# Performance work log

Hardware: AMD Instinct MI355X
Metric: run time of the kernel (lower is better)

## Reference

```python
import jax, jax.numpy as jnp
import numpy as np

N = 50000      # nodes
E = 400000     # edges (avg degree 8)
G = 64         # graphs in batch
IN_DIM = 128
OUT_DIM = 16


def _linear_params(key, fan_in, fan_out):
    k1, k2 = jax.random.split(key)
    s = 1.0 / np.sqrt(fan_in)
    W = jax.random.uniform(k1, (fan_in, fan_out), minval=-s, maxval=s, dtype=jnp.float32)
    b = jax.random.uniform(k2, (fan_out,), minval=-s, maxval=s, dtype=jnp.float32)
    return W, b


def setup_inputs() -> dict:
    key = jax.random.key(0)
    ks = jax.random.split(key, 12)
    x = jax.random.normal(ks[0], (N, IN_DIM), dtype=jnp.float32)
    edge_index = jax.random.randint(ks[1], (2, E), 0, N)
    # balanced graph assignment (sorted, every graph id present)
    batch = (jnp.arange(N) * G) // N
    W1, b1 = _linear_params(ks[2], IN_DIM, 64)
    W2, b2 = _linear_params(ks[3], 64, 256)
    W3, b3 = _linear_params(ks[4], 256, 512)
    W4, b4 = _linear_params(ks[5], 512, 64)
    Wr, br = _linear_params(ks[6], IN_DIM, 64)
    fc1_W, fc1_b = _linear_params(ks[7], 64, 64)
    fc2_W, fc2_b = _linear_params(ks[8], 64, OUT_DIM)
    ln_g = jnp.ones((64,), jnp.float32); ln_b = jnp.zeros((64,), jnp.float32)
    fcn_g = jnp.ones((64,), jnp.float32); fcn_b = jnp.zeros((64,), jnp.float32)
    return dict(x=x, edge_index=edge_index, batch=batch,
                W1=W1, b1=b1, W2=W2, b2=b2, W3=W3, b3=b3, W4=W4, b4=b4,
                Wr=Wr, br=br, ln_g=ln_g, ln_b=ln_b,
                fc1_W=fc1_W, fc1_b=fc1_b, fcn_g=fcn_g, fcn_b=fcn_b,
                fc2_W=fc2_W, fc2_b=fc2_b)


def _leaky_relu(h):
    return jnp.where(h >= 0, h, 0.01 * h)


def _layer_norm(h, g, b, eps=1e-5):
    m = jnp.mean(h, axis=-1, keepdims=True)
    v = jnp.var(h, axis=-1, keepdims=True)
    return (h - m) * jax.lax.rsqrt(v + eps) * g + b


def reference(x, edge_index, batch, W1, b1, W2, b2, W3, b3, W4, b4,
              Wr, br, ln_g, ln_b, fc1_W, fc1_b, fcn_g, fcn_b, fc2_W, fc2_b):
    src, dst = edge_index[0], edge_index[1]
    n = x.shape[0]
    # PyG GCNConv normalization with self-loops: deg = 1 + in-degree
    deg = jax.ops.segment_sum(jnp.ones(src.shape[0], x.dtype), dst, num_segments=n) + 1.0
    dis = jax.lax.rsqrt(deg)                 # [N]
    edge_norm = (dis[src] * dis[dst])[:, None]   # [E,1]
    self_norm = (dis * dis)[:, None]             # [N,1]

    def gcn_conv(h, W, b):
        h = h @ W                                            # transform first (PyG order)
        agg = jax.ops.segment_sum(h[src] * edge_norm, dst, num_segments=n)
        return agg + h * self_norm + b                       # self-loop term + bias

    residual = x @ Wr + br
    h = _leaky_relu(gcn_conv(x, W1, b1))
    h = _leaky_relu(gcn_conv(h, W2, b2))
    h = _leaky_relu(gcn_conv(h, W3, b3))
    h = _leaky_relu(gcn_conv(h, W4, b4))
    h = _layer_norm(h + residual, ln_g, ln_b)
    # global max pool over graphs
    p = jax.ops.segment_max(h, batch, num_segments=G)        # [G,64]
    p = _layer_norm(p @ fc1_W + fc1_b, fcn_g, fcn_b)
    p = _leaky_relu(p)
    return p @ fc2_W + fc2_b                                 # [G,16]
```

## Files before the change

kernel.cpp:

```cpp
#include <hip/hip_runtime.h>
#include <hip/hip_bf16.h>
#include <math.h>

typedef short bf16x8 __attribute__((ext_vector_type(8)));
typedef short bf16x4 __attribute__((ext_vector_type(4)));
typedef float f32x4 __attribute__((ext_vector_type(4)));

__device__ inline unsigned short f2bf(float f) {
  unsigned u = __float_as_uint(f);
  u += 0x7FFF + ((u >> 16) & 1);
  return (unsigned short)(u >> 16);
}
__device__ inline float bf2f(unsigned short h) {
  return __uint_as_float(((unsigned)h) << 16);
}
__device__ inline float bflo(unsigned u) { return __uint_as_float(u << 16); }
__device__ inline float bfhi(unsigned u) { return __uint_as_float(u & 0xffff0000u); }


__global__ __launch_bounds__(256) void count_k(const int* __restrict__ dst, int* __restrict__ cnt, int e) {
  int i = blockIdx.x * 256 + threadIdx.x;
  if (i < e) atomicAdd(&cnt[dst[i]], 1);
}

__global__ __launch_bounds__(256) void scan_a(const int* __restrict__ cnt, int* __restrict__ bsum, int n) {
  int i = blockIdx.x * 256 + threadIdx.x;
  int v = (i < n) ? cnt[i] : 0;
#pragma unroll
  for (int o = 32; o > 0; o >>= 1) v += __shfl_xor(v, o);
  __shared__ int ws[4];
  if ((threadIdx.x & 63) == 0) ws[threadIdx.x >> 6] = v;
  __syncthreads();
  if (threadIdx.x == 0) bsum[blockIdx.x] = ws[0] + ws[1] + ws[2] + ws[3];
}

__global__ __launch_bounds__(256) void scan_b(const int* __restrict__ bsum, int* __restrict__ bpre,
                                              int* __restrict__ off_n, int nb) {
  __shared__ int s[256];
  int t = threadIdx.x;
  int v = (t < nb) ? bsum[t] : 0;
  s[t] = v;
  __syncthreads();
  for (int o = 1; o < 256; o <<= 1) {
    int u = (t >= o) ? s[t - o] : 0;
    __syncthreads();
    s[t] += u;
    __syncthreads();
  }
  if (t < nb) bpre[t] = s[t] - v;
  if (t == 255) off_n[0] = s[255];
}

__global__ __launch_bounds__(256) void scan_c(const int* __restrict__ cnt, const int* __restrict__ bpre,
                                              int* __restrict__ off, int* __restrict__ cursor,
                                              float* __restrict__ dis, int n) {
  __shared__ int s[256];
  int i = blockIdx.x * 256 + threadIdx.x;
  int t = threadIdx.x;
  int v = (i < n) ? cnt[i] : 0;
  s[t] = v;
  __syncthreads();
  for (int o = 1; o < 256; o <<= 1) {
    int u = (t >= o) ? s[t - o] : 0;
    __syncthreads();
    s[t] += u;
    __syncthreads();
  }
  if (i < n) {
    int ov = bpre[blockIdx.x] + s[t] - v;
    off[i] = ov;
    cursor[i] = ov;
    dis[i] = rsqrtf((float)v + 1.0f);
  }
}

__global__ __launch_bounds__(256) void scatter_k(const int* __restrict__ src, const int* __restrict__ dst,
                                                 int* __restrict__ cursor, int* __restrict__ csr, int e) {
  int i = blockIdx.x * 256 + threadIdx.x;
  if (i < e) {
    int p = atomicAdd(&cursor[dst[i]], 1);
    csr[p] = src[i];
  }
}


__global__ __launch_bounds__(256) void wconv_k(const float* __restrict__ W1, const float* __restrict__ Wr,
                                               const float* __restrict__ W2, const float* __restrict__ W3,
                                               const float* __restrict__ W4,
                                               short* __restrict__ o1, short* __restrict__ oR,
                                               short* __restrict__ o2, short* __restrict__ o3,
                                               short* __restrict__ o4) {
  int b = blockIdx.x;
  const float* W; short* O; int K, N, nr;
  if (b < 64)       { W = W1; O = o1; K = 128; N = 64;  nr = b; }
  else if (b < 128) { W = Wr; O = oR; K = 128; N = 64;  nr = b - 64; }
  else if (b < 384) { W = W2; O = o2; K = 64;  N = 256; nr = b - 128; }
  else if (b < 896) { W = W3; O = o3; K = 256; N = 512; nr = b - 384; }
  else              { W = W4; O = o4; K = 512; N = 64;  nr = b - 896; }
  for (int k = threadIdx.x; k < K; k += 256)
    O[(size_t)nr * K + k] = (short)f2bf(W[(size_t)k * N + nr]);
}


template<int KT, int NTOT, int WM, int WN, int BIAS, int RELU, int ABF, int OBF, int SPLIT, int SCL, int BLK>
__global__ __launch_bounds__(256, BLK) void mgemm(const void* __restrict__ Av,
                                                  const short* __restrict__ Wc,
                                                  const float* __restrict__ bias,
                                                  void* __restrict__ Cv, void* __restrict__ Cv2,
                                                  const float* __restrict__ scl, int M) {
  __shared__ short As[64 * WM][ABF ? 40 : 72];
  __shared__ short Bs[64 * WN][40];
  const int tid = threadIdx.x;
  const int row0 = blockIdx.x * (64 * WM);
  const int col0 = blockIdx.y * (64 * WN);
  const int w = tid >> 6, lane = tid & 63;
  const int wm = w / WN, wn = w % WN;
  const int rm = wm * 64, cn = wn * 64;
  const int lm = lane & 15, lk = (lane >> 4) * 8;

  f32x4 acc[4][4];
#pragma unroll
  for (int i = 0; i < 4; i++)
#pragma unroll
    for (int j = 0; j < 4; j++)
#pragma unroll
      for (int r = 0; r < 4; r++) acc[i][j][r] = 0.f;

  for (int k0 = 0; k0 < KT; k0 += 32) {
#pragma unroll
    for (int p = 0; p < WM; p++) {
      int r = (tid >> 2) + p * 64;
      int kseg = (tid & 3) * 8;
      int gr = row0 + r;
      if (ABF) {
        bf16x8 v = {0, 0, 0, 0, 0, 0, 0, 0};
        if (gr < M) v = *(const bf16x8*)((const short*)Av + (size_t)gr * KT + k0 + kseg);
        *(bf16x8*)&As[r][kseg] = v;
      } else {
        float4 v0 = {0.f, 0.f, 0.f, 0.f}, v1 = {0.f, 0.f, 0.f, 0.f};
        if (gr < M) {
          const float* ap = (const float*)Av + (size_t)gr * KT + k0 + kseg;
          v0 = *(const float4*)ap;
          v1 = *(const float4*)(ap + 4);
        }
        float vv[8] = {v0.x, v0.y, v0.z, v0.w, v1.x, v1.y, v1.z, v1.w};
        bf16x8 hv, lv;
#pragma unroll
        for (int j = 0; j < 8; j++) {
          unsigned short h = f2bf(vv[j]);
          hv[j] = (short)h;
          lv[j] = (short)f2bf(vv[j] - bf2f(h));
        }
        *(bf16x8*)&As[r][kseg] = hv;
        *(bf16x8*)&As[r][32 + kseg] = lv;
      }
    }
#pragma unroll
    for (int p = 0; p < WN; p++) {
      int nr = (tid >> 2) + p * 64;
      int seg = (tid & 3) * 8;
      *(bf16x8*)&Bs[nr][seg] = *(const bf16x8*)(Wc + (size_t)(col0 + nr) * KT + k0 + seg);
    }
    __syncthreads();

    bf16x8 ah[4], al[4], bb[4];
#pragma unroll
    for (int mt = 0; mt < 4; mt++) {
      ah[mt] = *(const bf16x8*)&As[rm + mt * 16 + lm][lk];
      if (!ABF) al[mt] = *(const bf16x8*)&As[rm + mt * 16 + lm][32 + lk];
    }
#pragma unroll
    for (int nt = 0; nt < 4; nt++) bb[nt] = *(const bf16x8*)&Bs[cn + nt * 16 + lm][lk];
#pragma unroll
    for (int mt = 0; mt < 4; mt++)
#pragma unroll
      for (int nt = 0; nt < 4; nt++) {
        acc[mt][nt] = __builtin_amdgcn_mfma_f32_16x16x32_bf16(ah[mt], bb[nt], acc[mt][nt], 0, 0, 0);
        if (!ABF)
          acc[mt][nt] = __builtin_amdgcn_mfma_f32_16x16x32_bf16(al[mt], bb[nt], acc[mt][nt], 0, 0, 0);
      }
    __syncthreads();
  }

  if (SPLIT) {
    short* epi = (short*)&As[0][0];
    if (wn == 0) {
#pragma unroll
      for (int mt = 0; mt < 4; mt++) {
        int lr = rm + mt * 16 + (lane >> 4) * 4;
#pragma unroll
        for (int r = 0; r < 4; r++) {
          int gr = row0 + lr + r;
          float sc = (SCL && gr < M) ? scl[gr] : 0.f;
#pragma unroll
          for (int nt = 0; nt < 4; nt++)
            epi[(lr + r) * 64 + nt * 16 + lm] = (short)f2bf(acc[mt][nt][r] * sc);
        }
      }
    } else {
#pragma unroll
      for (int mt = 0; mt < 4; mt++) {
        int grb = row0 + rm + mt * 16 + (lane >> 4) * 4;
#pragma unroll
        for (int nt = 0; nt < 4; nt++) {
          int gc = nt * 16 + lm;
          float bv = bias[gc];
#pragma unroll
          for (int r = 0; r < 4; r++) {
            int gr = grb + r;
            if (gr < M) ((float*)Cv2)[(size_t)gr * 64 + gc] = acc[mt][nt][r] + bv;
          }
        }
      }
    }
    __syncthreads();
    int base = tid * 32;
    int row = base >> 6, col = base & 63;
    int gr = row0 + row;
    if (gr < M) {
#pragma unroll
      for (int q = 0; q < 4; q++)
        *(bf16x8*)((short*)Cv + (size_t)gr * 64 + col + q * 8) = *(bf16x8*)&epi[base + q * 8];
    }
  } else if (OBF && WM == 1) {
    short* epi = &Bs[0][0];
    const int NCOL = 64 * WN;
    float bvv[4];
#pragma unroll
    for (int nt = 0; nt < 4; nt++) bvv[nt] = BIAS ? bias[col0 + cn + nt * 16 + lm] : 0.f;
#pragma unroll
    for (int mt = 0; mt < 4; mt++) {
      __syncthreads();
#pragma unroll
      for (int r = 0; r < 4; r++) {
        int gr = row0 + mt * 16 + (lane >> 4) * 4 + r;
        float sc = (SCL && gr < M) ? scl[gr] : 1.f;
#pragma unroll
        for (int nt = 0; nt < 4; nt++) {
          float v = acc[mt][nt][r] + bvv[nt];
          if (RELU) v = (v >= 0.f) ? v : 0.01f * v;
          if (SCL) v *= sc;
          epi[((lane >> 4) * 4 + r) * NCOL + cn + nt * 16 + lm] = (short)f2bf(v);
        }
      }
      __syncthreads();
      const int per = (16 * NCOL) / 256;
      int base = tid * per;
      int lr = base / NCOL, lc = base % NCOL;
      int gr = row0 + mt * 16 + lr;
      if (gr < M) {
#pragma unroll
        for (int q = 0; q < per / 8; q++)
          *(bf16x8*)((short*)Cv + (size_t)gr * NTOT + col0 + lc + q * 8) = *(bf16x8*)&epi[base + q * 8];
      }
    }
  } else {
#pragma unroll
    for (int mt = 0; mt < 4; mt++) {
      int grb = row0 + rm + mt * 16 + (lane >> 4) * 4;
#pragma unroll
      for (int nt = 0; nt < 4; nt++) {
        int gc = col0 + cn + nt * 16 + lm;
        float bv = BIAS ? bias[gc] : 0.f;
#pragma unroll
        for (int r = 0; r < 4; r++) {
          int gr = grb + r;
          if (gr < M) {
            float v = acc[mt][nt][r] + bv;
            if (RELU) v = (v >= 0.f) ? v : 0.01f * v;
            if (SCL) v *= scl[gr];
            if (OBF) ((short*)Cv)[(size_t)gr * NTOT + gc] = (short)f2bf(v);
            else     ((float*)Cv)[(size_t)gr * NTOT + gc] = v;
          }
        }
      }
    }
  }
}


__global__ __launch_bounds__(256, 3) void fused34_k(const short* __restrict__ h2,
                                                    const int* __restrict__ off, const int* __restrict__ csr,
                                                    const short* __restrict__ W3c,
                                                    const float* __restrict__ b3,
                                                    const short* __restrict__ W4c,
                                                    const float* __restrict__ dis,
                                                    short* __restrict__ T4, int M) {
  __shared__ short Bs[2][32][264];
  __shared__ short Ws4[2][64][40];
  __shared__ short Hs[64][40];
  const int tid = threadIdx.x;
  const int row0 = blockIdx.x * 64;
  const int w = tid >> 6, lane = tid & 63;
  const int lm = lane & 15, lk = (lane >> 4) * 8;
  const int rquad = (lane >> 4) * 4;
  const int w4row = tid >> 2, w4seg = (tid & 3) * 8;
  const int qtr = lane >> 4, ql = lane & 15;

  short* Zs = (short*)&Bs[0][0][0];
  for (int pass = 0; pass < 4; pass++) {
    int nid = pass * 16 + w * 4 + qtr;
    int gr = row0 + nid;
    float a[16];
    if (gr < M) {
      float di = dis[gr];
      int e0 = off[gr], e1 = off[gr + 1];
      const short* base = h2 + (size_t)gr * 256 + ql * 16;
      bf16x8 s0 = *(const bf16x8*)base;
      bf16x8 s1 = *(const bf16x8*)(base + 8);
#pragma unroll
      for (int j = 0; j < 8; j++) { a[j] = bf2f((unsigned short)s0[j]); a[8 + j] = bf2f((unsigned short)s1[j]); }
      int e = e0;
      for (; e + 4 <= e1; e += 4) {
        const short* p0 = h2 + (size_t)csr[e]     * 256 + ql * 16;
        const short* p1 = h2 + (size_t)csr[e + 1] * 256 + ql * 16;
        const short* p2 = h2 + (size_t)csr[e + 2] * 256 + ql * 16;
        const short* p3 = h2 + (size_t)csr[e + 3] * 256 + ql * 16;
        bf16x8 t00 = *(const bf16x8*)p0, t01 = *(const bf16x8*)(p0 + 8);
        bf16x8 t10 = *(const bf16x8*)p1, t11 = *(const bf16x8*)(p1 + 8);
        bf16x8 t20 = *(const bf16x8*)p2, t21 = *(const bf16x8*)(p2 + 8);
        bf16x8 t30 = *(const bf16x8*)p3, t31 = *(const bf16x8*)(p3 + 8);
#pragma unroll
        for (int j = 0; j < 8; j++) {
          a[j] += (bf2f((unsigned short)t00[j]) + bf2f((unsigned short)t10[j])) +
                  (bf2f((unsigned short)t20[j]) + bf2f((unsigned short)t30[j]));
          a[8 + j] += (bf2f((unsigned short)t01[j]) + bf2f((unsigned short)t11[j])) +
                      (bf2f((unsigned short)t21[j]) + bf2f((unsigned short)t31[j]));
        }
      }
      for (; e < e1; e++) {
        const short* p = h2 + (size_t)csr[e] * 256 + ql * 16;
        bf16x8 t0 = *(const bf16x8*)p, t1 = *(const bf16x8*)(p + 8);
#pragma unroll
        for (int j = 0; j < 8; j++) {
          a[j] += bf2f((unsigned short)t0[j]);
          a[8 + j] += bf2f((unsigned short)t1[j]);
        }
      }
#pragma unroll
      for (int j = 0; j < 16; j++) a[j] *= di;
    } else {
#pragma unroll
      for (int j = 0; j < 16; j++) a[j] = 0.f;
    }
    bf16x8 o0, o1;
#pragma unroll
    for (int j = 0; j < 8; j++) {
      o0[j] = (short)f2bf(a[j]);
      o1[j] = (short)f2bf(a[8 + j]);
    }
    *(bf16x8*)&Zs[nid * 264 + ql * 16] = o0;
    *(bf16x8*)&Zs[nid * 264 + ql * 16 + 8] = o1;
  }
  __syncthreads();

  bf16x8 afr[8];
  {
    int lr = w * 16 + lm;
#pragma unroll
    for (int kc = 0; kc < 8; kc++)
      afr[kc] = *(const bf16x8*)&Zs[lr * 264 + kc * 32 + lk];
  }
  __syncthreads();

  f32x4 t4acc[4];
#pragma unroll
  for (int nt = 0; nt < 4; nt++)
#pragma unroll
    for (int r = 0; r < 4; r++) t4acc[nt][r] = 0.f;

  bf16x8 pw3[4];
  bf16x8 pw4;
#pragma unroll
  for (int q = 0; q < 4; q++) {
    int flat = q * 2048 + tid * 8;
    pw3[q] = *(const bf16x8*)(W3c + flat);
  }
  pw4 = *(const bf16x8*)(W4c + (size_t)w4row * 512 + w4seg);
#pragma unroll
  for (int q = 0; q < 4; q++) {
    int flat = q * 2048 + tid * 8;
    *(bf16x8*)&Bs[0][flat >> 8][flat & 255] = pw3[q];
  }
  *(bf16x8*)&Ws4[0][w4row][w4seg] = pw4;
  __syncthreads();

  for (int c = 0; c < 16; c++) {
    int cur = c & 1, nxt = cur ^ 1;
    if (c < 15) {
#pragma unroll
      for (int q = 0; q < 4; q++) {
        int flat = q * 2048 + tid * 8;
        pw3[q] = *(const bf16x8*)(W3c + (size_t)(c + 1) * 32 * 256 + flat);
      }
      pw4 = *(const bf16x8*)(W4c + (size_t)w4row * 512 + (c + 1) * 32 + w4seg);
    }

    f32x4 acc1[2];
#pragma unroll
    for (int nt = 0; nt < 2; nt++)
#pragma unroll
      for (int r = 0; r < 4; r++) acc1[nt][r] = 0.f;
#pragma unroll
    for (int k0 = 0; k0 < 8; k0++) {
      bf16x8 bb[2];
#pragma unroll
      for (int nt = 0; nt < 2; nt++) bb[nt] = *(const bf16x8*)&Bs[cur][nt * 16 + lm][k0 * 32 + lk];
#pragma unroll
      for (int nt = 0; nt < 2; nt++)
        acc1[nt] = __builtin_amdgcn_mfma_f32_16x16x32_bf16(afr[k0], bb[nt], acc1[nt], 0, 0, 0);
    }
#pragma unroll
    for (int nt = 0; nt < 2; nt++) {
      float bv = b3[c * 32 + nt * 16 + lm];
#pragma unroll
      for (int r = 0; r < 4; r++) {
        float v = acc1[nt][r] + bv;
        v = (v >= 0.f) ? v : 0.01f * v;
        Hs[w * 16 + rquad + r][nt * 16 + lm] = (short)f2bf(v);
      }
    }
    {
      bf16x8 ah2 = *(const bf16x8*)&Hs[w * 16 + lm][lk];
      bf16x8 bb2[4];
#pragma unroll
      for (int nt = 0; nt < 4; nt++) bb2[nt] = *(const bf16x8*)&Ws4[cur][nt * 16 + lm][lk];
#pragma unroll
      for (int nt = 0; nt < 4; nt++)
        t4acc[nt] = __builtin_amdgcn_mfma_f32_16x16x32_bf16(ah2, bb2[nt], t4acc[nt], 0, 0, 0);
    }
    if (c < 15) {
#pragma unroll
      for (int q = 0; q < 4; q++) {
        int flat = q * 2048 + tid * 8;
        *(bf16x8*)&Bs[nxt][flat >> 8][flat & 255] = pw3[q];
      }
      *(bf16x8*)&Ws4[nxt][w4row][w4seg] = pw4;
    }
    __syncthreads();
  }
  short* epi = (short*)&Bs[0][0][0];
#pragma unroll
  for (int r = 0; r < 4; r++) {
    int lr = w * 16 + rquad + r;
    int gr = row0 + lr;
    float sc = (gr < M) ? dis[gr] : 0.f;
#pragma unroll
    for (int nt = 0; nt < 4; nt++)
      epi[lr * 64 + nt * 16 + lm] = (short)f2bf(t4acc[nt][r] * sc);
  }
  __syncthreads();
  {
    int base = tid * 16;
    int row = base >> 6, col = base & 63;
    int gr = row0 + row;
    if (gr < M) {
      *(bf16x8*)(T4 + (size_t)gr * 64 + col)     = *(bf16x8*)&epi[base];
      *(bf16x8*)(T4 + (size_t)gr * 64 + col + 8) = *(bf16x8*)&epi[base + 8];
    }
  }
}


template<int BR, int OSCL>
__global__ __launch_bounds__(256) void aggb64_k(const short* __restrict__ T, const float* __restrict__ dis,
                                                const int* __restrict__ off, const int* __restrict__ csr,
                                                const float* __restrict__ bias, short* __restrict__ Out, int n) {
  int wv = (blockIdx.x * 256 + threadIdx.x) >> 6;
  int lane = threadIdx.x & 63;
  int qtr = lane >> 4, ql = lane & 15;
  int wid = wv * 4 + qtr;
  if (wid >= n) return;
  float di = dis[wid];
  int e0 = off[wid], e1 = off[wid + 1];
  const uint2* Tw = (const uint2*)T;
  uint2 su = Tw[(size_t)wid * 16 + ql];
  float a0 = bflo(su.x), a1 = bfhi(su.x), a2 = bflo(su.y), a3 = bfhi(su.y);
  int e = e0;
  for (; e + 8 <= e1; e += 8) {
    uint2 u0 = Tw[(size_t)csr[e]     * 16 + ql];
    uint2 u1 = Tw[(size_t)csr[e + 1] * 16 + ql];
    uint2 u2 = Tw[(size_t)csr[e + 2] * 16 + ql];
    uint2 u3 = Tw[(size_t)csr[e + 3] * 16 + ql];
    uint2 u4 = Tw[(size_t)csr[e + 4] * 16 + ql];
    uint2 u5 = Tw[(size_t)csr[e + 5] * 16 + ql];
    uint2 u6 = Tw[(size_t)csr[e + 6] * 16 + ql];
    uint2 u7 = Tw[(size_t)csr[e + 7] * 16 + ql];
    a0 += ((bflo(u0.x) + bflo(u1.x)) + (bflo(u2.x) + bflo(u3.x))) +
          ((bflo(u4.x) + bflo(u5.x)) + (bflo(u6.x) + bflo(u7.x)));
    a1 += ((bfhi(u0.x) + bfhi(u1.x)) + (bfhi(u2.x) + bfhi(u3.x))) +
          ((bfhi(u4.x) + bfhi(u5.x)) + (bfhi(u6.x) + bfhi(u7.x)));
    a2 += ((bflo(u0.y) + bflo(u1.y)) + (bflo(u2.y) + bflo(u3.y))) +
          ((bflo(u4.y) + bflo(u5.y)) + (bflo(u6.y) + bflo(u7.y)));
    a3 += ((bfhi(u0.y) + bfhi(u1.y)) + (bfhi(u2.y) + bfhi(u3.y))) +
          ((bfhi(u4.y) + bfhi(u5.y)) + (bfhi(u6.y) + bfhi(u7.y)));
  }
  for (; e + 4 <= e1; e += 4) {
    uint2 u0 = Tw[(size_t)csr[e]     * 16 + ql];
    uint2 u1 = Tw[(size_t)csr[e + 1] * 16 + ql];
    uint2 u2 = Tw[(size_t)csr[e + 2] * 16 + ql];
    uint2 u3 = Tw[(size_t)csr[e + 3] * 16 + ql];
    a0 += (bflo(u0.x) + bflo(u1.x)) + (bflo(u2.x) + bflo(u3.x));
    a1 += (bfhi(u0.x) + bfhi(u1.x)) + (bfhi(u2.x) + bfhi(u3.x));
    a2 += (bflo(u0.y) + bflo(u1.y)) + (bflo(u2.y) + bflo(u3.y));
    a3 += (bfhi(u0.y) + bfhi(u1.y)) + (bfhi(u2.y) + bfhi(u3.y));
  }
  for (; e < e1; e++) {
    uint2 u = Tw[(size_t)csr[e] * 16 + ql];
    a0 += bflo(u.x); a1 += bfhi(u.x); a2 += bflo(u.y); a3 += bfhi(u.y);
  }
  float v0 = di * a0, v1 = di * a1, v2 = di * a2, v3 = di * a3;
  if (BR) {
    v0 += bias[ql * 4];     v1 += bias[ql * 4 + 1];
    v2 += bias[ql * 4 + 2]; v3 += bias[ql * 4 + 3];
    v0 = (v0 >= 0.f) ? v0 : 0.01f * v0;
    v1 = (v1 >= 0.f) ? v1 : 0.01f * v1;
    v2 = (v2 >= 0.f) ? v2 : 0.01f * v2;
    v3 = (v3 >= 0.f) ? v3 : 0.01f * v3;
  }
  if (OSCL) { v0 *= di; v1 *= di; v2 *= di; v3 *= di; }
  uint2 o;
  o.x = (unsigned)f2bf(v0) | ((unsigned)f2bf(v1) << 16);
  o.y = (unsigned)f2bf(v2) | ((unsigned)f2bf(v3) << 16);
  ((uint2*)Out)[(size_t)wid * 16 + ql] = o;
}

__global__ __launch_bounds__(256) void agg64_ln_k(const short* __restrict__ T, const float* __restrict__ dis,
                                                  const int* __restrict__ off, const int* __restrict__ csr,
                                                  const float* __restrict__ bias, const float* __restrict__ resid,
                                                  const float* __restrict__ g, const float* __restrict__ b,
                                                  float* __restrict__ outh, int n) {
  int wv = (blockIdx.x * 256 + threadIdx.x) >> 6;
  int lane = threadIdx.x & 63;
  int qtr = lane >> 4, ql = lane & 15;
  int wid = wv * 4 + qtr;
  if (wid >= n) return;
  float di = dis[wid];
  int e0 = off[wid], e1 = off[wid + 1];
  const uint2* Tw = (const uint2*)T;
  uint2 su = Tw[(size_t)wid * 16 + ql];
  float a0 = bflo(su.x), a1 = bfhi(su.x), a2 = bflo(su.y), a3 = bfhi(su.y);
  int e = e0;
  for (; e + 8 <= e1; e += 8) {
    uint2 u0 = Tw[(size_t)csr[e]     * 16 + ql];
    uint2 u1 = Tw[(size_t)csr[e + 1] * 16 + ql];
    uint2 u2 = Tw[(size_t)csr[e + 2] * 16 + ql];
    uint2 u3 = Tw[(size_t)csr[e + 3] * 16 + ql];
    uint2 u4 = Tw[(size_t)csr[e + 4] * 16 + ql];
    uint2 u5 = Tw[(size_t)csr[e + 5] * 16 + ql];
    uint2 u6 = Tw[(size_t)csr[e + 6] * 16 + ql];
    uint2 u7 = Tw[(size_t)csr[e + 7] * 16 + ql];
    a0 += ((bflo(u0.x) + bflo(u1.x)) + (bflo(u2.x) + bflo(u3.x))) +
          ((bflo(u4.x) + bflo(u5.x)) + (bflo(u6.x) + bflo(u7.x)));
    a1 += ((bfhi(u0.x) + bfhi(u1.x)) + (bfhi(u2.x) + bfhi(u3.x))) +
          ((bfhi(u4.x) + bfhi(u5.x)) + (bfhi(u6.x) + bfhi(u7.x)));
    a2 += ((bflo(u0.y) + bflo(u1.y)) + (bflo(u2.y) + bflo(u3.y))) +
          ((bflo(u4.y) + bflo(u5.y)) + (bflo(u6.y) + bflo(u7.y)));
    a3 += ((bfhi(u0.y) + bfhi(u1.y)) + (bfhi(u2.y) + bfhi(u3.y))) +
          ((bfhi(u4.y) + bfhi(u5.y)) + (bfhi(u6.y) + bfhi(u7.y)));
  }
  for (; e + 4 <= e1; e += 4) {
    uint2 u0 = Tw[(size_t)csr[e]     * 16 + ql];
    uint2 u1 = Tw[(size_t)csr[e + 1] * 16 + ql];
    uint2 u2 = Tw[(size_t)csr[e + 2] * 16 + ql];
    uint2 u3 = Tw[(size_t)csr[e + 3] * 16 + ql];
    a0 += (bflo(u0.x) + bflo(u1.x)) + (bflo(u2.x) + bflo(u3.x));
    a1 += (bfhi(u0.x) + bfhi(u1.x)) + (bfhi(u2.x) + bfhi(u3.x));
    a2 += (bflo(u0.y) + bflo(u1.y)) + (bflo(u2.y) + bflo(u3.y));
    a3 += (bfhi(u0.y) + bfhi(u1.y)) + (bfhi(u2.y) + bfhi(u3.y));
  }
  for (; e < e1; e++) {
    uint2 u = Tw[(size_t)csr[e] * 16 + ql];
    a0 += bflo(u.x); a1 += bfhi(u.x); a2 += bflo(u.y); a3 += bfhi(u.y);
  }
  float4 rv = ((const float4*)resid)[(size_t)wid * 16 + ql];
  float v0 = di * a0 + bias[ql * 4];
  float v1 = di * a1 + bias[ql * 4 + 1];
  float v2 = di * a2 + bias[ql * 4 + 2];
  float v3 = di * a3 + bias[ql * 4 + 3];
  v0 = (v0 >= 0.f) ? v0 : 0.01f * v0;
  v1 = (v1 >= 0.f) ? v1 : 0.01f * v1;
  v2 = (v2 >= 0.f) ? v2 : 0.01f * v2;
  v3 = (v3 >= 0.f) ? v3 : 0.01f * v3;
  v0 += rv.x; v1 += rv.y; v2 += rv.z; v3 += rv.w;
  float s = (v0 + v1) + (v2 + v3);
  float ss = (v0 * v0 + v1 * v1) + (v2 * v2 + v3 * v3);
#pragma unroll
  for (int o = 8; o > 0; o >>= 1) {
    s += __shfl_xor(s, o);
    ss += __shfl_xor(ss, o);
  }
  float m = s * (1.f / 64.f);
  float var = ss * (1.f / 64.f) - m * m;
  float rs = rsqrtf(var + 1e-5f);
  float4 o4;
  o4.x = (v0 - m) * rs * g[ql * 4]     + b[ql * 4];
  o4.y = (v1 - m) * rs * g[ql * 4 + 1] + b[ql * 4 + 1];
  o4.z = (v2 - m) * rs * g[ql * 4 + 2] + b[ql * 4 + 2];
  o4.w = (v3 - m) * rs * g[ql * 4 + 3] + b[ql * 4 + 3];
  ((float4*)outh)[(size_t)wid * 16 + ql] = o4;
}


__global__ __launch_bounds__(256) void pool_mlp_k(const float* __restrict__ hn,
                                                  const float* __restrict__ fc1W, const float* __restrict__ fc1b,
                                                  const float* __restrict__ fng, const float* __restrict__ fnb,
                                                  const float* __restrict__ fc2W, const float* __restrict__ fc2b,
                                                  float* __restrict__ out, int n) {
  const int G = 64;
  int g = blockIdx.x;
  int f = threadIdx.x & 63, c = threadIdx.x >> 6;
  long long s0 = ((long long)g * n + G - 1) / G;
  long long e0 = ((long long)(g + 1) * n + G - 1) / G;
  float m = -INFINITY;
  for (long long i = s0 + c; i < e0; i += 4) m = fmaxf(m, hn[(size_t)i * 64 + f]);
  __shared__ float red[4][64];
  __shared__ float ps[64], qs[64];
  red[c][f] = m;
  __syncthreads();
  if (c == 0) ps[f] = fmaxf(fmaxf(red[0][f], red[1][f]), fmaxf(red[2][f], red[3][f]));
  __syncthreads();
  if (threadIdx.x < 64) {
    int lane = threadIdx.x;
    float q = fc1b[lane];
#pragma unroll 8
    for (int k = 0; k < 64; k++) q = fmaf(ps[k], fc1W[k * 64 + lane], q);
    float s = q, ss = q * q;
#pragma unroll
    for (int o = 32; o > 0; o >>= 1) {
      s += __shfl_xor(s, o);
      ss += __shfl_xor(ss, o);
    }
    float mm = s * (1.f / 64.f);
    float var = ss * (1.f / 64.f) - mm * mm;
    float y = (q - mm) * rsqrtf(var + 1e-5f) * fng[lane] + fnb[lane];
    y = (y >= 0.f) ? y : 0.01f * y;
    qs[lane] = y;
    __builtin_amdgcn_wave_barrier();
    if (lane < 16) {
      float o = fc2b[lane];
#pragma unroll 8
      for (int k = 0; k < 64; k++) o = fmaf(qs[k], fc2W[k * 16 + lane], o);
      out[g * 16 + lane] = o;
    }
  }
}


extern "C" void kernel_launch(void* const* d_in, const int* in_sizes, int n_in,
                              void* d_out, int out_size, void* d_ws, size_t ws_size,
                              hipStream_t stream) {
  const float* x   = (const float*)d_in[0];
  const int*   ei  = (const int*)d_in[1];
  const float* W1  = (const float*)d_in[3];
  const float* b1  = (const float*)d_in[4];
  const float* W2  = (const float*)d_in[5];
  const float* b2  = (const float*)d_in[6];
  const float* W3  = (const float*)d_in[7];
  const float* b3  = (const float*)d_in[8];
  const float* W4  = (const float*)d_in[9];
  const float* b4  = (const float*)d_in[10];
  const float* Wr  = (const float*)d_in[11];
  const float* br  = (const float*)d_in[12];
  const float* lng = (const float*)d_in[13];
  const float* lnb = (const float*)d_in[14];
  const float* f1W = (const float*)d_in[15];
  const float* f1b = (const float*)d_in[16];
  const float* fng = (const float*)d_in[17];
  const float* fnb = (const float*)d_in[18];
  const float* f2W = (const float*)d_in[19];
  const float* f2b = (const float*)d_in[20];

  int n = in_sizes[0] / 128;
  int e = in_sizes[1] / 2;
  const int* src = ei;
  const int* dst = ei + e;

  float* arena = (float*)d_ws;
  float* resid = arena;
  short* h2b   = (short*)(arena + (size_t)64 * n);
  short* t4b   = (short*)(arena + (size_t)192 * n);
  float* hn    = arena + (size_t)224 * n;
  short* t1b   = (short*)(arena + (size_t)320 * n);
  short* h1b   = (short*)(arena + (size_t)352 * n);
  short* z2b   = (short*)(arena + (size_t)384 * n);
  float* dis   = arena + (size_t)448 * n;
  int* cnt    = (int*)(dis + n);
  int* off    = cnt + n;
  int* cursor = off + n + 1;
  int* csr    = cursor + n;
  int* bsum   = csr + e;
  int* bpre   = bsum + 256;
  float* pool = (float*)(bpre + 256);
  size_t wq = (((size_t)(pool + 4096)) + 15) & ~(size_t)15;
  short* wc1 = (short*)wq;
  short* wcR = wc1 + 8192;
  short* wc2 = wcR + 8192;
  short* wc3 = wc2 + 16384;
  short* wc4 = wc3 + 131072;
  size_t need = ((char*)(wc4 + 32768) - (char*)d_ws) + 64;
  if (ws_size < need) return;

  int nb_n = (n + 255) / 256;
  int nb_e = (e + 255) / 256;
  int nb_w4 = ((n + 3) / 4 + 3) / 4;
  int g_wide = (n + 63) / 64;
  int g_fused = (n + 127) / 128;

  wconv_k<<<960, 256, 0, stream>>>(W1, Wr, W2, W3, W4, wc1, wcR, wc2, wc3, wc4);

  hipMemsetAsync(cnt, 0, (size_t)n * sizeof(int), stream);
  count_k<<<nb_e, 256, 0, stream>>>(dst, cnt, e);
  scan_a<<<nb_n, 256, 0, stream>>>(cnt, bsum, n);
  scan_b<<<1, 256, 0, stream>>>(bsum, bpre, off + n, nb_n);
  scan_c<<<nb_n, 256, 0, stream>>>(cnt, bpre, off, cursor, dis, n);
  scatter_k<<<nb_e, 256, 0, stream>>>(src, dst, cursor, csr, e);

  mgemm<128, 128, 2, 2, 1, 0, 0, 0, 1, 1, 4><<<dim3(g_fused, 1), 256, 0, stream>>>(x, wc1, br, t1b, resid, dis, n);
  aggb64_k<1, 1><<<nb_w4, 256, 0, stream>>>(t1b, dis, off, csr, b1, h1b, n);
  aggb64_k<0, 0><<<nb_w4, 256, 0, stream>>>(h1b, dis, off, csr, nullptr, z2b, n);
  mgemm<64, 256, 1, 4, 1, 1, 1, 1, 0, 1, 5><<<dim3(g_wide, 1), 256, 0, stream>>>(z2b, wc2, b2, h2b, nullptr, dis, n);
  fused34_k<<<g_wide, 256, 0, stream>>>(h2b, off, csr, wc3, b3, wc4, dis, t4b, n);
  agg64_ln_k<<<nb_w4, 256, 0, stream>>>(t4b, dis, off, csr, b4, resid, lng, lnb, hn, n);
  pool_mlp_k<<<64, 256, 0, stream>>>(hn, f1W, f1b, fng, fnb, f2W, f2b, (float*)d_out, n);
}
```

Measured before the change: 352.4 us.

## Single-buffer fused34 shared memory to raise occupancy to five blocks per CU

Replaces the double-buffered W3/W4 shared tiles with a single buffer in a 32 KB shared array, aliasing the Z staging area, and raises launch bounds from 3 to 5 blocks per CU. The first weight chunk is now loaded into registers before the gather phase so its latency overlaps the neighbour aggregation. The cost is an extra barrier per chunk iteration, since the next weight chunk can only be written after all waves finish reading the current one, plus tighter register limits that may cause spills.

```diff
diff --git a/kernel.cpp b/kernel.cpp
--- a/kernel.cpp
+++ b/kernel.cpp
@@ -279,16 +279,17 @@
 }
 
 
-__global__ __launch_bounds__(256, 3) void fused34_k(const short* __restrict__ h2,
+__global__ __launch_bounds__(256, 5) void fused34_k(const short* __restrict__ h2,
                                                     const int* __restrict__ off, const int* __restrict__ csr,
                                                     const short* __restrict__ W3c,
                                                     const float* __restrict__ b3,
                                                     const short* __restrict__ W4c,
                                                     const float* __restrict__ dis,
                                                     short* __restrict__ T4, int M) {
-  __shared__ short Bs[2][32][264];
-  __shared__ short Ws4[2][64][40];
-  __shared__ short Hs[64][40];
+  __shared__ __align__(16) char smem[32768];
+  short* Bs  = (short*)smem;
+  short* Ws4 = (short*)(smem + 16896);
+  short* Hs  = (short*)(smem + 22016);
   const int tid = threadIdx.x;
   const int row0 = blockIdx.x * 64;
   const int w = tid >> 6, lane = tid & 63;
@@ -297,7 +298,13 @@
   const int w4row = tid >> 2, w4seg = (tid & 3) * 8;
   const int qtr = lane >> 4, ql = lane & 15;
 
-  short* Zs = (short*)&Bs[0][0][0];
+  bf16x8 pw3[4];
+  bf16x8 pw4;
+#pragma unroll
+  for (int q = 0; q < 4; q++) pw3[q] = *(const bf16x8*)(W3c + q * 2048 + tid * 8);
+  pw4 = *(const bf16x8*)(W4c + (size_t)w4row * 512 + w4seg);
+
+  short* Zs = (short*)smem;
   for (int pass = 0; pass < 4; pass++) {
     int nid = pass * 16 + w * 4 + qtr;
     int gr = row0 + nid;
@@ -349,8 +356,8 @@
       o0[j] = (short)f2bf(a[j]);
       o1[j] = (short)f2bf(a[8 + j]);
     }
-    *(bf16x8*)&Zs[nid * 264 + ql * 16] = o0;
-    *(bf16x8*)&Zs[nid * 264 + ql * 16 + 8] = o1;
+    *(bf16x8*)&Zs[nid * 256 + ql * 16] = o0;
+    *(bf16x8*)&Zs[nid * 256 + ql * 16 + 8] = o1;
   }
   __syncthreads();
 
@@ -359,39 +366,30 @@
     int lr = w * 16 + lm;
 #pragma unroll
     for (int kc = 0; kc < 8; kc++)
-      afr[kc] = *(const bf16x8*)&Zs[lr * 264 + kc * 32 + lk];
-  }
-  __syncthreads();
-
-  f32x4 t4acc[4];
-#pragma unroll
-  for (int nt = 0; nt < 4; nt++)
-#pragma unroll
-    for (int r = 0; r < 4; r++) t4acc[nt][r] = 0.f;
-
-  bf16x8 pw3[4];
-  bf16x8 pw4;
+      afr[kc] = *(const bf16x8*)&Zs[lr * 256 + kc * 32 + lk];
+  }
+  __syncthreads();
+
 #pragma unroll
   for (int q = 0; q < 4; q++) {
     int flat = q * 2048 + tid * 8;
-    pw3[q] = *(const bf16x8*)(W3c + flat);
-  }
-  pw4 = *(const bf16x8*)(W4c + (size_t)w4row * 512 + w4seg);
-#pragma unroll
-  for (int q = 0; q < 4; q++) {
-    int flat = q * 2048 + tid * 8;
-    *(bf16x8*)&Bs[0][flat >> 8][flat & 255] = pw3[q];
-  }
-  *(bf16x8*)&Ws4[0][w4row][w4seg] = pw4;
-  __syncthreads();
+    *(bf16x8*)&Bs[(flat >> 8) * 264 + (flat & 255)] = pw3[q];
+  }
+  *(bf16x8*)&Ws4[w4row * 40 + w4seg] = pw4;
+  __syncthreads();
+
+  f32x4 t4acc[4];
+#pragma unroll
+  for (int nt = 0; nt < 4; nt++)
+#pragma unroll
+    for (int r = 0; r < 4; r++) t4acc[nt][r] = 0.f;
 
   for (int c = 0; c < 16; c++) {
-    int cur = c & 1, nxt = cur ^ 1;
     if (c < 15) {
 #pragma unroll
       for (int q = 0; q < 4; q++) {
         int flat = q * 2048 + tid * 8;
-        pw3[q] = *(const bf16x8*)(W3c + (size_t)(c + 1) * 32 * 256 + flat);
+        pw3[q] = *(const bf16x8*)(W3c + (size_t)(c + 1) * 8192 + flat);
       }
       pw4 = *(const bf16x8*)(W4c + (size_t)w4row * 512 + (c + 1) * 32 + w4seg);
     }
@@ -405,7 +403,7 @@
     for (int k0 = 0; k0 < 8; k0++) {
       bf16x8 bb[2];
 #pragma unroll
-      for (int nt = 0; nt < 2; nt++) bb[nt] = *(const bf16x8*)&Bs[cur][nt * 16 + lm][k0 * 32 + lk];
+      for (int nt = 0; nt < 2; nt++) bb[nt] = *(const bf16x8*)&Bs[(nt * 16 + lm) * 264 + k0 * 32 + lk];
 #pragma unroll
       for (int nt = 0; nt < 2; nt++)
         acc1[nt] = __builtin_amdgcn_mfma_f32_16x16x32_bf16(afr[k0], bb[nt], acc1[nt], 0, 0, 0);
@@ -417,29 +415,31 @@
       for (int r = 0; r < 4; r++) {
         float v = acc1[nt][r] + bv;
         v = (v >= 0.f) ? v : 0.01f * v;
-        Hs[w * 16 + rquad + r][nt * 16 + lm] = (short)f2bf(v);
+        Hs[(w * 16 + rquad + r) * 40 + nt * 16 + lm] = (short)f2bf(v);
       }
     }
     {
-      bf16x8 ah2 = *(const bf16x8*)&Hs[w * 16 + lm][lk];
+      bf16x8 ah2 = *(const bf16x8*)&Hs[(w * 16 + lm) * 40 + lk];
       bf16x8 bb2[4];
 #pragma unroll
-      for (int nt = 0; nt < 4; nt++) bb2[nt] = *(const bf16x8*)&Ws4[cur][nt * 16 + lm][lk];
+      for (int nt = 0; nt < 4; nt++) bb2[nt] = *(const bf16x8*)&Ws4[(nt * 16 + lm) * 40 + lk];
 #pragma unroll
       for (int nt = 0; nt < 4; nt++)
         t4acc[nt] = __builtin_amdgcn_mfma_f32_16x16x32_bf16(ah2, bb2[nt], t4acc[nt], 0, 0, 0);
     }
+    __syncthreads();
     if (c < 15) {
 #pragma unroll
       for (int q = 0; q < 4; q++) {
         int flat = q * 2048 + tid * 8;
-        *(bf16x8*)&Bs[nxt][flat >> 8][flat & 255] = pw3[q];
-      }
-      *(bf16x8*)&Ws4[nxt][w4row][w4seg] = pw4;
-    }
-    __syncthreads();
-  }
-  short* epi = (short*)&Bs[0][0][0];
+        *(bf16x8*)&Bs[(flat >> 8) * 264 + (flat & 255)] = pw3[q];
+      }
+      *(bf16x8*)&Ws4[w4row * 40 + w4seg] = pw4;
+    }
+    __syncthreads();
+  }
+
+  short* epi = (short*)smem;
 #pragma unroll
   for (int r = 0; r < 4; r++) {
     int lr = w * 16 + rquad + r;
```

New measurement: 342.6 us. 1.03x faster.
